# Optimization experiments

Measured on AMD Instinct MI355X. Metric: run time of the kernel, lower is better.

The kernel has to match this reference:

```python
import jax, jax.numpy as jnp
import numpy as np

N_NODES = 50000
N_EDGES = 800000
N_FEAT = 128
N_HID = 128
N_CLASS = 40


def _mean_aggregate(x, src, dst, num_nodes):
    # PyG 'mean' aggregation: for each target node, mean of source-neighbor features.
    msgs = x[src]                                             # [E, D] gather
    sums = jax.ops.segment_sum(msgs, dst, num_segments=num_nodes)   # [N, D]
    ones = jnp.ones((src.shape[0],), dtype=x.dtype)
    cnt = jax.ops.segment_sum(ones, dst, num_segments=num_nodes)    # [N]
    return sums / jnp.maximum(cnt, 1.0)[:, None]


def setup_inputs() -> dict:
    key = jax.random.key(0)
    ks = jax.random.split(key, 8)
    x = jax.random.normal(ks[0], (N_NODES, N_FEAT), dtype=jnp.float32)
    edge_index = jax.random.randint(ks[1], (2, N_EDGES), 0, N_NODES, dtype=jnp.int64)
    s1 = 1.0 / np.sqrt(N_FEAT)
    s2 = 1.0 / np.sqrt(N_HID)
    return {
        "x": x,
        "edge_index": edge_index,
        # SAGEConv 1: lin_l acts on aggregated neighbors (has bias), lin_r on root (no bias)
        "Wl1": jax.random.normal(ks[2], (N_FEAT, N_HID), dtype=jnp.float32) * s1,
        "Wr1": jax.random.normal(ks[3], (N_FEAT, N_HID), dtype=jnp.float32) * s1,
        "b1": jnp.zeros((N_HID,), dtype=jnp.float32),
        # SAGEConv 2 (gc2)
        "Wl2": jax.random.normal(ks[4], (N_HID, N_CLASS), dtype=jnp.float32) * s2,
        "Wr2": jax.random.normal(ks[5], (N_HID, N_CLASS), dtype=jnp.float32) * s2,
        "b2": jnp.zeros((N_CLASS,), dtype=jnp.float32),
    }


def reference(x, edge_index, Wl1, Wr1, b1, Wl2, Wr2, b2):
    src, dst = edge_index[0], edge_index[1]
    n = x.shape[0]
    # Layer 1: SAGEConv -> relu (dropout is identity in eval mode)
    agg = _mean_aggregate(x, src, dst, n)                 # [N, F]
    h = jax.nn.relu(agg @ Wl1 + x @ Wr1 + b1)             # [N, H]
    # Layer 2: SAGEConv (logits)
    agg2 = _mean_aggregate(h, src, dst, n)                # [N, H]
    out = agg2 @ Wl2 + h @ Wr2 + b2                       # [N, C]
    return out
```

## Files before the change

kernel.cpp:

```cpp
#include <hip/hip_runtime.h>
#include <hip/hip_bf16.h>

#define N_FEAT 128
#define N_HID  128
#define N_CLASS 40

#define NP   256
#define PSZ  196
#define BCAP 4096
#define BCHUNK 4096

#define HSTRIDE 136

typedef __attribute__((ext_vector_type(8))) __bf16 bf16x8;
typedef __attribute__((ext_vector_type(4))) float f32x4;

__device__ __forceinline__ unsigned short f2bf(float f) {
    union { float f; unsigned int u; } v; v.f = f;
    unsigned int r = (v.u + 0x7FFFu + ((v.u >> 16) & 1u)) >> 16;
    return (unsigned short)r;
}
__device__ __forceinline__ float bf2f_lo(unsigned int p) {
    union { unsigned int u; float f; } v; v.u = p << 16; return v.f;
}
__device__ __forceinline__ float bf2f_hi(unsigned int p) {
    union { unsigned int u; float f; } v; v.u = p & 0xFFFF0000u; return v.f;
}

__device__ __forceinline__ void swz_body(const float* __restrict__ W,
                                         unsigned short* __restrict__ sw,
                                         int ncols, int t, int nt) {
    if (t >= nt * 4 * 64) return;
    int lane = t & 63;
    int bi = t >> 6;
    int kc = bi & 3, ct = bi >> 2;
    int n = lane & 15, q = lane >> 4;
    int col = ct * 16 + n;
    #pragma unroll
    for (int j = 0; j < 8; ++j) {
        int k = kc * 32 + q * 8 + j;
        float f = (col < ncols) ? W[(size_t)k * ncols + col] : 0.f;
        sw[(size_t)t * 8 + j] = f2bf(f);
    }
}
__device__ __forceinline__ void swzc_body(const float* __restrict__ Wl2,
                                          const float* __restrict__ Wr2,
                                          unsigned short* __restrict__ sw, int t) {
    if (t >= 5 * 4 * 64) return;
    int lane = t & 63;
    int bi = t >> 6;
    int kc = bi & 3, ct = bi >> 2;
    int n = lane & 15, q = lane >> 4;
    int col = ct * 16 + n;
    #pragma unroll
    for (int j = 0; j < 8; ++j) {
        int k = kc * 32 + q * 8 + j;
        float f = (col < N_CLASS) ? Wl2[(size_t)k * N_CLASS + col]
                                  : Wr2[(size_t)k * N_CLASS + (col - N_CLASS)];
        sw[(size_t)t * 8 + j] = f2bf(f);
    }
}

__global__ __launch_bounds__(256) void k_prep(const float* __restrict__ x,
                                              unsigned short* __restrict__ xb, int nCvt, int nElem,
                                              const float* __restrict__ Wl1,
                                              const float* __restrict__ Wr1,
                                              const float* __restrict__ Wl2,
                                              const float* __restrict__ Wr2,
                                              unsigned short* __restrict__ w1l,
                                              unsigned short* __restrict__ w1r,
                                              unsigned short* __restrict__ wc,
                                              int* __restrict__ ptail) {
    int b = blockIdx.x, t = threadIdx.x;
    if (b < nCvt) {
        int i = (b * 256 + t) * 4;
        if (i < nElem) {
            float4 v = *(const float4*)(x + i);
            ushort4 o;
            o.x = f2bf(v.x); o.y = f2bf(v.y); o.z = f2bf(v.z); o.w = f2bf(v.w);
            *(ushort4*)(xb + i) = o;
        }
        return;
    }
    b -= nCvt;
    if (b < 8) { swz_body(Wl1, w1l, N_HID, b * 256 + t, 8); return; }
    b -= 8;
    if (b < 8) { swz_body(Wr1, w1r, N_HID, b * 256 + t, 8); return; }
    b -= 8;
    if (b < 5) { swzc_body(Wl2, Wr2, wc, b * 256 + t); return; }
    ptail[t] = 0;
}

__global__ __launch_bounds__(256) void k_bin(const int* __restrict__ src,
                                             const int* __restrict__ dst,
                                             int* __restrict__ ptail,
                                             uint2* __restrict__ bins, int E) {
    __shared__ uint2 stage[BCHUNK];
    __shared__ int lcnt[NP], lofs[NP], lcur[NP], gbase[NP];
    __shared__ int ws4[4];
    int t = threadIdx.x;
    int base = blockIdx.x * BCHUNK;
    int nE = min(BCHUNK, E - base);
    lcnt[t] = 0;
    __syncthreads();
    for (int i = t; i < nE; i += 256) {
        int d = dst[base + i];
        atomicAdd(&lcnt[d / PSZ], 1);
    }
    __syncthreads();
    {
        int v = lcnt[t];
        int lane = t & 63, wid = t >> 6;
        int inc = v;
        #pragma unroll
        for (int s = 1; s < 64; s <<= 1) {
            int u = __shfl_up(inc, s);
            if (lane >= s) inc += u;
        }
        if (lane == 63) ws4[wid] = inc;
        __syncthreads();
        int wb = 0;
        for (int w = 0; w < wid; ++w) wb += ws4[w];
        int exc = wb + inc - v;
        lofs[t] = exc;
        lcur[t] = exc;
        gbase[t] = atomicAdd(&ptail[t], v);
    }
    __syncthreads();
    for (int i = t; i < nE; i += 256) {
        int d = dst[base + i];
        int s = src[base + i];
        int pos = atomicAdd(&lcur[d / PSZ], 1);
        stage[pos] = make_uint2((unsigned)s, (unsigned)d);
    }
    __syncthreads();
    for (int i = t; i < nE; i += 256) {
        uint2 pr = stage[i];
        int p = (int)pr.y / PSZ;
        bins[(size_t)p * BCAP + gbase[p] + (i - lofs[p])] = pr;
    }
}

__global__ __launch_bounds__(256) void k_pscan(const int* __restrict__ ptail,
                                               int* __restrict__ pbase,
                                               int* __restrict__ off, int N) {
    int t = threadIdx.x;
    int lane = t & 63, wid = t >> 6;
    int v = ptail[t];
    int inc = v;
    #pragma unroll
    for (int s = 1; s < 64; s <<= 1) {
        int u = __shfl_up(inc, s);
        if (lane >= s) inc += u;
    }
    __shared__ int ws[4];
    if (lane == 63) ws[wid] = inc;
    __syncthreads();
    int wb = 0;
    for (int w = 0; w < wid; ++w) wb += ws[w];
    pbase[t] = wb + inc - v;
    if (t == NP - 1) off[N] = wb + inc;
}

__global__ __launch_bounds__(256) void k_build(const uint2* __restrict__ bins,
                                               const int* __restrict__ ptail,
                                               const int* __restrict__ pbase,
                                               int* __restrict__ off,
                                               int* __restrict__ srt, int N) {
    int p = blockIdx.x;
    __shared__ int lc[256], lofs[256];
    __shared__ int ws4[4];
    int t = threadIdx.x;
    lc[t] = 0;
    __syncthreads();
    int n = ptail[p];
    const uint2* bp = bins + (size_t)p * BCAP;
    for (int i = t; i < n; i += 256)
        atomicAdd(&lc[(int)bp[i].y - p * PSZ], 1);
    __syncthreads();
    {
        int v = lc[t];
        int lane = t & 63, wid = t >> 6;
        int inc = v;
        #pragma unroll
        for (int s = 1; s < 64; s <<= 1) {
            int u = __shfl_up(inc, s);
            if (lane >= s) inc += u;
        }
        if (lane == 63) ws4[wid] = inc;
        __syncthreads();
        int wb = 0;
        for (int w = 0; w < wid; ++w) wb += ws4[w];
        lofs[t] = pbase[p] + wb + inc - v;
    }
    __syncthreads();
    int g = p * PSZ + t;
    if (t < PSZ && g < N) off[g] = lofs[t];
    __syncthreads();
    for (int i = t; i < n; i += 256) {
        uint2 pr = bp[i];
        int pos = atomicAdd(&lofs[(int)pr.y - p * PSZ], 1);
        srt[pos] = (int)pr.x;
    }
}

__global__ __launch_bounds__(256) void k_aggb4(const unsigned short* __restrict__ feat,
                                               const int* __restrict__ srt,
                                               const int* __restrict__ off,
                                               unsigned short* __restrict__ outp, int n_nodes) {
    int wave = (blockIdx.x * blockDim.x + threadIdx.x) >> 6;
    int lane = threadIdx.x & 63;
    if (wave >= n_nodes) return;
    int q = lane >> 4;
    int l = lane & 15;
    int beg = off[wave];
    int end = off[wave + 1];
    float a0 = 0.f, a1 = 0.f, a2 = 0.f, a3 = 0.f,
          a4 = 0.f, a5 = 0.f, a6 = 0.f, a7 = 0.f;
    int e = beg + q;
    #define ACCUM128(P) { \
        a0 += bf2f_lo(P.x); a1 += bf2f_hi(P.x); \
        a2 += bf2f_lo(P.y); a3 += bf2f_hi(P.y); \
        a4 += bf2f_lo(P.z); a5 += bf2f_hi(P.z); \
        a6 += bf2f_lo(P.w); a7 += bf2f_hi(P.w); }
    for (; e + 4 < end; e += 8) {
        int s0 = srt[e];
        int s1 = srt[e + 4];
        uint4 p0 = *(const uint4*)(feat + (size_t)s0 * N_FEAT + l * 8);
        uint4 p1 = *(const uint4*)(feat + (size_t)s1 * N_FEAT + l * 8);
        ACCUM128(p0)
        ACCUM128(p1)
    }
    if (e < end) {
        int s0 = srt[e];
        uint4 p0 = *(const uint4*)(feat + (size_t)s0 * N_FEAT + l * 8);
        ACCUM128(p0)
    }
    #undef ACCUM128
    #define RED(A) A += __shfl_xor(A, 16); A += __shfl_xor(A, 32);
    RED(a0) RED(a1) RED(a2) RED(a3) RED(a4) RED(a5) RED(a6) RED(a7)
    #undef RED
    if (q == 0) {
        int c = end - beg;
        float inv = 1.0f / (float)(c > 1 ? c : 1);
        uint4 o;
        o.x = ((unsigned int)f2bf(a1 * inv) << 16) | f2bf(a0 * inv);
        o.y = ((unsigned int)f2bf(a3 * inv) << 16) | f2bf(a2 * inv);
        o.z = ((unsigned int)f2bf(a5 * inv) << 16) | f2bf(a4 * inv);
        o.w = ((unsigned int)f2bf(a7 * inv) << 16) | f2bf(a6 * inv);
        *(uint4*)(outp + (size_t)wave * N_FEAT + l * 8) = o;
    }
}

__global__ __launch_bounds__(256) void k_gemm12(const unsigned short* __restrict__ aggb,
                                                const unsigned short* __restrict__ xb,
                                                const unsigned short* __restrict__ Bl,
                                                const unsigned short* __restrict__ Br,
                                                const float* __restrict__ bias1,
                                                const unsigned short* __restrict__ Bc,
                                                const float* __restrict__ bias2,
                                                unsigned short* __restrict__ p2b,
                                                float* __restrict__ r2, int n_nodes) {
    __shared__ unsigned short hlds[4][16 * HSTRIDE];
    int tid = threadIdx.x;
    int wv = tid >> 6;
    int wid = (blockIdx.x * 256 + tid) >> 6;
    int lane = tid & 63;
    int nb = wid * 16;
    if (nb >= n_nodes) return;
    int m = lane & 15, q = lane >> 4;
    size_t abase = (size_t)(nb + m) * N_FEAT + q * 8;
    bf16x8 Aa0 = *(const bf16x8*)(aggb + abase);
    bf16x8 Aa1 = *(const bf16x8*)(aggb + abase + 32);
    bf16x8 Aa2 = *(const bf16x8*)(aggb + abase + 64);
    bf16x8 Aa3 = *(const bf16x8*)(aggb + abase + 96);
    bf16x8 Ax0 = *(const bf16x8*)(xb + abase);
    bf16x8 Ax1 = *(const bf16x8*)(xb + abase + 32);
    bf16x8 Ax2 = *(const bf16x8*)(xb + abase + 64);
    bf16x8 Ax3 = *(const bf16x8*)(xb + abase + 96);
    const bf16x8* blp = (const bf16x8*)Bl + lane;
    const bf16x8* brp = (const bf16x8*)Br + lane;
    unsigned short* hl = hlds[wv];

    #pragma unroll
    for (int ct = 0; ct < 8; ++ct) {
        f32x4 acc = {0.f, 0.f, 0.f, 0.f};
        acc = __builtin_amdgcn_mfma_f32_16x16x32_bf16(Aa0, blp[(ct*4+0)*64], acc, 0,0,0);
        acc = __builtin_amdgcn_mfma_f32_16x16x32_bf16(Ax0, brp[(ct*4+0)*64], acc, 0,0,0);
        acc = __builtin_amdgcn_mfma_f32_16x16x32_bf16(Aa1, blp[(ct*4+1)*64], acc, 0,0,0);
        acc = __builtin_amdgcn_mfma_f32_16x16x32_bf16(Ax1, brp[(ct*4+1)*64], acc, 0,0,0);
        acc = __builtin_amdgcn_mfma_f32_16x16x32_bf16(Aa2, blp[(ct*4+2)*64], acc, 0,0,0);
        acc = __builtin_amdgcn_mfma_f32_16x16x32_bf16(Ax2, brp[(ct*4+2)*64], acc, 0,0,0);
        acc = __builtin_amdgcn_mfma_f32_16x16x32_bf16(Aa3, blp[(ct*4+3)*64], acc, 0,0,0);
        acc = __builtin_amdgcn_mfma_f32_16x16x32_bf16(Ax3, brp[(ct*4+3)*64], acc, 0,0,0);
        int col = ct * 16 + m;
        float bv = bias1[col];
        hl[(q*4 + 0) * HSTRIDE + col] = f2bf(fmaxf(acc.x + bv, 0.f));
        hl[(q*4 + 1) * HSTRIDE + col] = f2bf(fmaxf(acc.y + bv, 0.f));
        hl[(q*4 + 2) * HSTRIDE + col] = f2bf(fmaxf(acc.z + bv, 0.f));
        hl[(q*4 + 3) * HSTRIDE + col] = f2bf(fmaxf(acc.w + bv, 0.f));
    }
    bf16x8 H0 = *(const bf16x8*)(hl + m * HSTRIDE + q * 8);
    bf16x8 H1 = *(const bf16x8*)(hl + m * HSTRIDE + q * 8 + 32);
    bf16x8 H2 = *(const bf16x8*)(hl + m * HSTRIDE + q * 8 + 64);
    bf16x8 H3 = *(const bf16x8*)(hl + m * HSTRIDE + q * 8 + 96);
    const bf16x8* bcp = (const bf16x8*)Bc + lane;

    #pragma unroll
    for (int ct = 0; ct < 5; ++ct) {
        f32x4 acc = {0.f, 0.f, 0.f, 0.f};
        acc = __builtin_amdgcn_mfma_f32_16x16x32_bf16(H0, bcp[(ct*4+0)*64], acc, 0,0,0);
        acc = __builtin_amdgcn_mfma_f32_16x16x32_bf16(H1, bcp[(ct*4+1)*64], acc, 0,0,0);
        acc = __builtin_amdgcn_mfma_f32_16x16x32_bf16(H2, bcp[(ct*4+2)*64], acc, 0,0,0);
        acc = __builtin_amdgcn_mfma_f32_16x16x32_bf16(H3, bcp[(ct*4+3)*64], acc, 0,0,0);
        int col = ct * 16 + m;
        if (col < N_CLASS) {
            p2b[(size_t)(nb + q*4 + 0) * N_CLASS + col] = f2bf(acc.x);
            p2b[(size_t)(nb + q*4 + 1) * N_CLASS + col] = f2bf(acc.y);
            p2b[(size_t)(nb + q*4 + 2) * N_CLASS + col] = f2bf(acc.z);
            p2b[(size_t)(nb + q*4 + 3) * N_CLASS + col] = f2bf(acc.w);
        } else {
            int rc = col - N_CLASS;
            float bv = bias2[rc];
            r2[(size_t)(nb + q*4 + 0) * N_CLASS + rc] = acc.x + bv;
            r2[(size_t)(nb + q*4 + 1) * N_CLASS + rc] = acc.y + bv;
            r2[(size_t)(nb + q*4 + 2) * N_CLASS + rc] = acc.z + bv;
            r2[(size_t)(nb + q*4 + 3) * N_CLASS + rc] = acc.w + bv;
        }
    }
}

__global__ __launch_bounds__(256) void k_agg40(const unsigned short* __restrict__ p2b,
                                               const float* __restrict__ r2,
                                               const int* __restrict__ srt,
                                               const int* __restrict__ off,
                                               float* __restrict__ outp, int n_nodes) {
    int wave = (blockIdx.x * blockDim.x + threadIdx.x) >> 6;
    int lane = threadIdx.x & 63;
    if (wave >= n_nodes) return;
    int q = lane >> 4;
    int l = lane & 15;
    bool act = l < 10;
    int beg = off[wave];
    int end = off[wave + 1];
    float a0 = 0.f, a1 = 0.f, a2 = 0.f, a3 = 0.f;
    int e = beg + q;
    #define ACCUM40(P) { \
        a0 += bf2f_lo(P.x); a1 += bf2f_hi(P.x); \
        a2 += bf2f_lo(P.y); a3 += bf2f_hi(P.y); }
    for (; e + 4 < end; e += 8) {
        int s0 = srt[e];
        int s1 = srt[e + 4];
        if (act) {
            uint2 p0 = *(const uint2*)(p2b + (size_t)s0 * N_CLASS + l * 4);
            uint2 p1 = *(const uint2*)(p2b + (size_t)s1 * N_CLASS + l * 4);
            ACCUM40(p0)
            ACCUM40(p1)
        }
    }
    if (e < end && act) {
        int s0 = srt[e];
        uint2 p0 = *(const uint2*)(p2b + (size_t)s0 * N_CLASS + l * 4);
        ACCUM40(p0)
    }
    #undef ACCUM40
    #define RED(A) A += __shfl_xor(A, 16); A += __shfl_xor(A, 32);
    RED(a0) RED(a1) RED(a2) RED(a3)
    #undef RED
    if (lane < 10) {
        int c = end - beg;
        float inv = 1.0f / (float)(c > 1 ? c : 1);
        float4 rr = *(const float4*)(r2 + (size_t)wave * N_CLASS + lane * 4);
        float4 o;
        o.x = fmaf(a0, inv, rr.x);
        o.y = fmaf(a1, inv, rr.y);
        o.z = fmaf(a2, inv, rr.z);
        o.w = fmaf(a3, inv, rr.w);
        *(float4*)(outp + (size_t)wave * N_CLASS + lane * 4) = o;
    }
}

extern "C" void kernel_launch(void* const* d_in, const int* in_sizes, int n_in,
                              void* d_out, int out_size, void* d_ws, size_t ws_size,
                              hipStream_t stream) {
    const float* x   = (const float*)d_in[0];
    const int*   ei  = (const int*)d_in[1];
    const float* Wl1 = (const float*)d_in[2];
    const float* Wr1 = (const float*)d_in[3];
    const float* b1  = (const float*)d_in[4];
    const float* Wl2 = (const float*)d_in[5];
    const float* Wr2 = (const float*)d_in[6];
    const float* b2  = (const float*)d_in[7];
    float* out = (float*)d_out;

    const int N = in_sizes[0] / N_FEAT;
    const int E = in_sizes[1] / 2;
    const int* src = ei;
    const int* dst = ei + E;

    unsigned short* xb   = (unsigned short*)d_ws;
    unsigned short* aggb = xb + (size_t)N * N_FEAT;
    unsigned short* p2b  = aggb + (size_t)N * N_FEAT;
    float* r2 = (float*)(p2b + (size_t)N * N_CLASS);
    uint2* bins = (uint2*)p2b;
    unsigned short* w1l  = (unsigned short*)(r2 + (size_t)N * N_CLASS);
    unsigned short* w1r  = w1l + 16384;
    unsigned short* wc   = w1r + 16384;
    int* off = (int*)(wc + 10240);
    int* srt = off + N + 1;
    int* ptail = srt + E;
    int* pbase = ptail + NP;

    const int TB = 256;
    int nCvt = (N * N_FEAT / 4 + TB - 1) / TB;
    int bblocks = (E + BCHUNK - 1) / BCHUNK;

    k_prep<<<nCvt + 8 + 8 + 5 + 1, TB, 0, stream>>>(x, xb, nCvt, N * N_FEAT,
                                                    Wl1, Wr1, Wl2, Wr2,
                                                    w1l, w1r, wc, ptail);
    k_bin<<<bblocks, TB, 0, stream>>>(src, dst, ptail, bins, E);
    k_pscan<<<1, TB, 0, stream>>>(ptail, pbase, off, N);
    k_build<<<NP, TB, 0, stream>>>(bins, ptail, pbase, off, srt, N);

    int aggblocks = (N * 64 + TB - 1) / TB;
    int gblocks = ((N + 15) / 16 + 3) / 4;

    k_aggb4<<<aggblocks, TB, 0, stream>>>(xb, srt, off, aggb, N);
    k_gemm12<<<gblocks, TB, 0, stream>>>(aggb, xb, w1l, w1r, b1, wc, b2, p2b, r2, N);
    k_agg40<<<aggblocks, TB, 0, stream>>>(p2b, r2, srt, off, out, N);
}
```

Baseline: 189.5 us.

## Fuse prep with edge binning, fold partition scan into build, unroll gathers

Merges the conversion/weight-swizzle kernel with the edge binning kernel into one launch, with the ptail reset moved to a memset. The single-block partition scan is dropped and each build block recomputes the 256-entry scan redundantly. The gather loops in both aggregation kernels are unrolled from 2 to 4 neighbors per quarter-wave to put more loads in flight. Together this cuts two kernel launches and their serialization, at the cost of more shared memory being allocated for the conversion blocks in the fused kernel, which may lower occupancy.

```diff
diff --git a/kernel.cpp b/kernel.cpp
--- a/kernel.cpp
+++ b/kernel.cpp
@@ -61,16 +61,20 @@
     }
 }
 
-__global__ __launch_bounds__(256) void k_prep(const float* __restrict__ x,
-                                              unsigned short* __restrict__ xb, int nCvt, int nElem,
-                                              const float* __restrict__ Wl1,
-                                              const float* __restrict__ Wr1,
-                                              const float* __restrict__ Wl2,
-                                              const float* __restrict__ Wr2,
-                                              unsigned short* __restrict__ w1l,
-                                              unsigned short* __restrict__ w1r,
-                                              unsigned short* __restrict__ wc,
-                                              int* __restrict__ ptail) {
+__global__ __launch_bounds__(256) void k_prepbin(const float* __restrict__ x,
+                                                 unsigned short* __restrict__ xb,
+                                                 int nCvt, int nElem,
+                                                 const float* __restrict__ Wl1,
+                                                 const float* __restrict__ Wr1,
+                                                 const float* __restrict__ Wl2,
+                                                 const float* __restrict__ Wr2,
+                                                 unsigned short* __restrict__ w1l,
+                                                 unsigned short* __restrict__ w1r,
+                                                 unsigned short* __restrict__ wc,
+                                                 const int* __restrict__ src,
+                                                 const int* __restrict__ dst,
+                                                 int* __restrict__ ptail,
+                                                 uint2* __restrict__ bins, int E) {
     int b = blockIdx.x, t = threadIdx.x;
     if (b < nCvt) {
         int i = (b * 256 + t) * 4;
@@ -88,18 +92,12 @@
     if (b < 8) { swz_body(Wr1, w1r, N_HID, b * 256 + t, 8); return; }
     b -= 8;
     if (b < 5) { swzc_body(Wl2, Wr2, wc, b * 256 + t); return; }
-    ptail[t] = 0;
-}
-
-__global__ __launch_bounds__(256) void k_bin(const int* __restrict__ src,
-                                             const int* __restrict__ dst,
-                                             int* __restrict__ ptail,
-                                             uint2* __restrict__ bins, int E) {
+    b -= 5;
+
     __shared__ uint2 stage[BCHUNK];
     __shared__ int lcnt[NP], lofs[NP], lcur[NP], gbase[NP];
     __shared__ int ws4[4];
-    int t = threadIdx.x;
-    int base = blockIdx.x * BCHUNK;
+    int base = b * BCHUNK;
     int nE = min(BCHUNK, E - base);
     lcnt[t] = 0;
     __syncthreads();
@@ -141,38 +139,34 @@
     }
 }
 
-__global__ __launch_bounds__(256) void k_pscan(const int* __restrict__ ptail,
-                                               int* __restrict__ pbase,
-                                               int* __restrict__ off, int N) {
-    int t = threadIdx.x;
-    int lane = t & 63, wid = t >> 6;
-    int v = ptail[t];
-    int inc = v;
-    #pragma unroll
-    for (int s = 1; s < 64; s <<= 1) {
-        int u = __shfl_up(inc, s);
-        if (lane >= s) inc += u;
-    }
-    __shared__ int ws[4];
-    if (lane == 63) ws[wid] = inc;
-    __syncthreads();
-    int wb = 0;
-    for (int w = 0; w < wid; ++w) wb += ws[w];
-    pbase[t] = wb + inc - v;
-    if (t == NP - 1) off[N] = wb + inc;
-}
-
 __global__ __launch_bounds__(256) void k_build(const uint2* __restrict__ bins,
                                                const int* __restrict__ ptail,
-                                               const int* __restrict__ pbase,
                                                int* __restrict__ off,
                                                int* __restrict__ srt, int N) {
     int p = blockIdx.x;
+    int t = threadIdx.x;
+    __shared__ int ws4[4];
+    __shared__ int sexc[NP];
     __shared__ int lc[256], lofs[256];
-    __shared__ int ws4[4];
-    int t = threadIdx.x;
+    {
+        int v = ptail[t];
+        int lane = t & 63, wid = t >> 6;
+        int inc = v;
+        #pragma unroll
+        for (int s = 1; s < 64; s <<= 1) {
+            int u = __shfl_up(inc, s);
+            if (lane >= s) inc += u;
+        }
+        if (lane == 63) ws4[wid] = inc;
+        __syncthreads();
+        int wb = 0;
+        for (int w = 0; w < wid; ++w) wb += ws4[w];
+        sexc[t] = wb + inc - v;
+        if (p == NP - 1 && t == NP - 1) off[N] = wb + inc;
+    }
     lc[t] = 0;
     __syncthreads();
+    int pb = sexc[p];
     int n = ptail[p];
     const uint2* bp = bins + (size_t)p * BCAP;
     for (int i = t; i < n; i += 256)
@@ -191,7 +185,7 @@
         __syncthreads();
         int wb = 0;
         for (int w = 0; w < wid; ++w) wb += ws4[w];
-        lofs[t] = pbase[p] + wb + inc - v;
+        lofs[t] = pb + wb + inc - v;
     }
     __syncthreads();
     int g = p * PSZ + t;
@@ -223,15 +217,21 @@
         a2 += bf2f_lo(P.y); a3 += bf2f_hi(P.y); \
         a4 += bf2f_lo(P.z); a5 += bf2f_hi(P.z); \
         a6 += bf2f_lo(P.w); a7 += bf2f_hi(P.w); }
-    for (; e + 4 < end; e += 8) {
+    for (; e + 12 < end; e += 16) {
         int s0 = srt[e];
         int s1 = srt[e + 4];
+        int s2 = srt[e + 8];
+        int s3 = srt[e + 12];
         uint4 p0 = *(const uint4*)(feat + (size_t)s0 * N_FEAT + l * 8);
         uint4 p1 = *(const uint4*)(feat + (size_t)s1 * N_FEAT + l * 8);
+        uint4 p2 = *(const uint4*)(feat + (size_t)s2 * N_FEAT + l * 8);
+        uint4 p3 = *(const uint4*)(feat + (size_t)s3 * N_FEAT + l * 8);
         ACCUM128(p0)
         ACCUM128(p1)
-    }
-    if (e < end) {
+        ACCUM128(p2)
+        ACCUM128(p3)
+    }
+    for (; e < end; e += 4) {
         int s0 = srt[e];
         uint4 p0 = *(const uint4*)(feat + (size_t)s0 * N_FEAT + l * 8);
         ACCUM128(p0)
@@ -348,20 +348,28 @@
     #define ACCUM40(P) { \
         a0 += bf2f_lo(P.x); a1 += bf2f_hi(P.x); \
         a2 += bf2f_lo(P.y); a3 += bf2f_hi(P.y); }
-    for (; e + 4 < end; e += 8) {
+    for (; e + 12 < end; e += 16) {
         int s0 = srt[e];
         int s1 = srt[e + 4];
+        int s2 = srt[e + 8];
+        int s3 = srt[e + 12];
         if (act) {
             uint2 p0 = *(const uint2*)(p2b + (size_t)s0 * N_CLASS + l * 4);
             uint2 p1 = *(const uint2*)(p2b + (size_t)s1 * N_CLASS + l * 4);
+            uint2 p2 = *(const uint2*)(p2b + (size_t)s2 * N_CLASS + l * 4);
+            uint2 p3 = *(const uint2*)(p2b + (size_t)s3 * N_CLASS + l * 4);
             ACCUM40(p0)
             ACCUM40(p1)
-        }
-    }
-    if (e < end && act) {
+            ACCUM40(p2)
+            ACCUM40(p3)
+        }
+    }
+    for (; e < end; e += 4) {
         int s0 = srt[e];
-        uint2 p0 = *(const uint2*)(p2b + (size_t)s0 * N_CLASS + l * 4);
-        ACCUM40(p0)
+        if (act) {
+            uint2 p0 = *(const uint2*)(p2b + (size_t)s0 * N_CLASS + l * 4);
+            ACCUM40(p0)
+        }
     }
     #undef ACCUM40
     #define RED(A) A += __shfl_xor(A, 16); A += __shfl_xor(A, 32);
@@ -409,18 +417,18 @@
     int* off = (int*)(wc + 10240);
     int* srt = off + N + 1;
     int* ptail = srt + E;
-    int* pbase = ptail + NP;
 
     const int TB = 256;
     int nCvt = (N * N_FEAT / 4 + TB - 1) / TB;
     int bblocks = (E + BCHUNK - 1) / BCHUNK;
 
-    k_prep<<<nCvt + 8 + 8 + 5 + 1, TB, 0, stream>>>(x, xb, nCvt, N * N_FEAT,
-                                                    Wl1, Wr1, Wl2, Wr2,
-                                                    w1l, w1r, wc, ptail);
-    k_bin<<<bblocks, TB, 0, stream>>>(src, dst, ptail, bins, E);
-    k_pscan<<<1, TB, 0, stream>>>(ptail, pbase, off, N);
-    k_build<<<NP, TB, 0, stream>>>(bins, ptail, pbase, off, srt, N);
+    hipMemsetAsync(ptail, 0, NP * sizeof(int), stream);
+
+    k_prepbin<<<nCvt + 21 + bblocks, TB, 0, stream>>>(x, xb, nCvt, N * N_FEAT,
+                                                      Wl1, Wr1, Wl2, Wr2,
+                                                      w1l, w1r, wc,
+                                                      src, dst, ptail, bins, E);
+    k_build<<<NP, TB, 0, stream>>>(bins, ptail, off, srt, N);
 
     int aggblocks = (N * 64 + TB - 1) / TB;
     int gblocks = ((N + 15) / 16 + 3) / 4;
```

Result: slower. 195.0 us (+2.9%).
